# Performance work log

Hardware: AMD Instinct MI355X
Metric: run time of the kernel (lower is better)

The kernel has to match this reference:

```python
import jax, jax.numpy as jnp
import numpy as np

DICT_LEN = 9
NUM_LS = 8
DIM = 1024
SEQ = 2048
BZ = 32


def setup_inputs() -> dict:
    key = jax.random.key(0)
    k_x, k_ids, k_w, k_b = jax.random.split(key, 4)
    x = jax.random.normal(k_x, (SEQ, BZ, DIM), dtype=jnp.float32)
    lang_ids = jax.random.randint(k_ids, (BZ,), 0, DICT_LEN)
    # torch nn.Linear init: U(-1/sqrt(in), 1/sqrt(in)), weight shape [out, in]
    bound = 1.0 / np.sqrt(DIM)
    W = jax.random.uniform(k_w, (NUM_LS, DIM, DIM), dtype=jnp.float32, minval=-bound, maxval=bound)
    b = jax.random.uniform(k_b, (NUM_LS, DIM), dtype=jnp.float32, minval=-bound, maxval=bound)
    return {"x": x, "lang_ids": lang_ids, "W": W, "b": b}


def reference(x, lang_ids, W, b):
    # Mapper.forward: gid = dict_len - 1 - lang_ids; tokens with gid in [1, num_ls]
    # are transformed by Linear #(gid-1); all other batch columns pass through.
    gid = DICT_LEN - 1 - lang_ids                      # [bz]
    active = (gid >= 1) & (gid <= NUM_LS)              # [bz]
    eidx = jnp.clip(gid - 1, 0, NUM_LS - 1)            # [bz] expert index (dummy 0 where inactive)
    We = W[eidx]                                       # [bz, dim, dim] (torch Linear weight layout [out, in])
    be = b[eidx]                                       # [bz, dim]
    y = jnp.einsum("sbd,bed->sbe", x, We) + be[None, :, :]
    return jnp.where(active[None, :, None], y, x)
```

## Files before the change

kernel.cpp:

```cpp
#include <hip/hip_runtime.h>
#include <hip/hip_bf16.h>

#define TSEQ 2048
#define TBZ  32
#define TDIM 1024
#define NLS  8

typedef __attribute__((ext_vector_type(8))) short bf16x8;
typedef __attribute__((ext_vector_type(4))) float f32x4;

__device__ inline unsigned int pk2(float lo, float hi) {
    __hip_bfloat162 h = __float22bfloat162_rn(make_float2(lo, hi));
    return *reinterpret_cast<const unsigned int*>(&h);
}

__device__ inline void gload_lds16(const void* g, void* l) {
    __builtin_amdgcn_global_load_lds(
        (const __attribute__((address_space(1))) unsigned int*)g,
        (__attribute__((address_space(3))) unsigned int*)l,
        16, 0, 0);
}

__global__ __launch_bounds__(256) void conv_x(const float* __restrict__ x,
                                              unsigned short* __restrict__ xb) {
    const int total = TSEQ * TBZ * TDIM / 8;
    const int stride = gridDim.x * 256;
    for (int i = blockIdx.x * 256 + threadIdx.x; i < total; i += stride) {
        const int d8  = i & (TDIM / 8 - 1);
        const int row = i >> 7;
        const int s   = row >> 5;
        const int b   = row & (TBZ - 1);
        const float* src = x + (long)row * TDIM + d8 * 8;
        f32x4 v0 = *(const f32x4*)(src);
        f32x4 v1 = *(const f32x4*)(src + 4);
        uint4 o;
        o.x = pk2(v0.x, v0.y); o.y = pk2(v0.z, v0.w);
        o.z = pk2(v1.x, v1.y); o.w = pk2(v1.z, v1.w);
        *(uint4*)(xb + (long)(b * TSEQ + s) * TDIM + d8 * 8) = o;
    }
}

__global__ __launch_bounds__(256) void conv_w(const float* __restrict__ W,
                                              unsigned short* __restrict__ wb) {
    const int total = NLS * TDIM * TDIM / 8;
    const int stride = gridDim.x * 256;
    for (int i = blockIdx.x * 256 + threadIdx.x; i < total; i += stride) {
        const float* src = W + (long)i * 8;
        f32x4 v0 = *(const f32x4*)(src);
        f32x4 v1 = *(const f32x4*)(src + 4);
        uint4 o;
        o.x = pk2(v0.x, v0.y); o.y = pk2(v0.z, v0.w);
        o.z = pk2(v1.x, v1.y); o.w = pk2(v1.z, v1.w);
        *(uint4*)(wb + (long)i * 8) = o;
    }
}


#define BAR __builtin_amdgcn_s_barrier()
#define LGKM asm volatile("s_waitcnt lgkmcnt(0)" ::: "memory")
#define VMC(n) asm volatile("s_waitcnt vmcnt(" #n ")" ::: "memory")

__global__ __launch_bounds__(512, 2) void mapper_gemm8(
    const unsigned short* __restrict__ xb,
    const int* __restrict__ lang_ids,
    const unsigned short* __restrict__ wb,
    const float* __restrict__ bias,
    const float* __restrict__ x,
    float* __restrict__ out)
{
    const int p  = blockIdx.x;
    const int l  = (p & 7) * 128 + (p >> 3);
    const int b  = l >> 5;
    const int mt = (l >> 2) & 7;
    const int nt = l & 3;
    const int s0 = mt * 256;
    const int e0 = nt * 256;
    const int tid = threadIdx.x;

    const int gid = 8 - lang_ids[b];
    const bool active = (gid >= 1) && (gid <= 8);
    int eb = gid - 1; eb = eb < 0 ? 0 : (eb > 7 ? 7 : eb);

    if (!active) {
        const f32x4* xs = (const f32x4*)x;
        f32x4*       os = (f32x4*)out;
        const int rs4 = TBZ * TDIM / 4;
        for (int i = tid; i < 256 * 256 / 4; i += 512) {
            int r = i >> 6;
            int c = i & 63;
            long idx = (long)(s0 + r) * rs4 + b * (TDIM / 4) + (e0 >> 2) + c;
            os[idx] = xs[idx];
        }
        return;
    }

    __shared__ uint4 ldsbuf[131072 / 16];
    char* ldsc = (char*)ldsbuf;

    const int lane = tid & 63;
    const int wave = tid >> 6;
    const int wr   = wave >> 2;
    const int wc   = wave & 3;
    const int fr   = lane & 15;
    const int fq   = lane >> 4;
    const int fr7  = fr & 7;

    const unsigned short* __restrict__ Aab = xb + (long)b  * TSEQ * TDIM + (long)s0 * TDIM;
    const unsigned short* __restrict__ Bbb = wb + (long)eb * TDIM * TDIM + (long)e0 * TDIM;

    const int L    = lane;
    const int lch8 = ((L & 7) ^ (L >> 3)) * 8;
    const int ldA0 = wave * 2048 + L * 16;
    const unsigned short* aG[2][2];
    const unsigned short* bG[2][2];
    #pragma unroll
    for (int j = 0; j < 2; ++j) {
        const int rr = wave * 16 + j * 8 + (L >> 3);
        #pragma unroll
        for (int mh = 0; mh < 2; ++mh)
            aG[j][mh] = Aab + ((rr >> 6) * 128 + mh * 64 + (rr & 63)) * TDIM + lch8;
        #pragma unroll
        for (int nh = 0; nh < 2; ++nh)
            bG[j][nh] = Bbb + ((rr >> 5) * 64 + nh * 32 + (rr & 31)) * TDIM + lch8;
    }

#define STAGE_A(slot, mh, kofs) do { \
    gload_lds16(aG[0][mh] + (kofs), ldsc + (slot)*32768 + (mh)*16384 + ldA0); \
    gload_lds16(aG[1][mh] + (kofs), ldsc + (slot)*32768 + (mh)*16384 + ldA0 + 1024); \
} while (0)
#define STAGE_B(slot, nh, kofs) do { \
    gload_lds16(bG[0][nh] + (kofs), ldsc + 65536 + (slot)*32768 + (nh)*16384 + ldA0); \
    gload_lds16(bG[1][nh] + (kofs), ldsc + 65536 + (slot)*32768 + (nh)*16384 + ldA0 + 1024); \
} while (0)
#define RD_A(slot, mh) do { \
    _Pragma("unroll") for (int ml = 0; ml < 4; ++ml) { \
        const int rr = wr * 64 + ml * 16 + fr; \
        _Pragma("unroll") for (int kk = 0; kk < 2; ++kk) \
            af[ml][kk] = *(const bf16x8*)(ldsc + (slot)*32768 + (mh)*16384 + rr*128 + (((kk*4+fq) ^ fr7) << 4)); \
    } } while (0)
#define RD_B(slot, nh, br) do { \
    _Pragma("unroll") for (int nl = 0; nl < 2; ++nl) { \
        const int rr = wc * 32 + nl * 16 + fr; \
        _Pragma("unroll") for (int kk = 0; kk < 2; ++kk) \
            br[nl][kk] = *(const bf16x8*)(ldsc + 65536 + (slot)*32768 + (nh)*16384 + rr*128 + (((kk*4+fq) ^ fr7) << 4)); \
    } } while (0)
#define MM(mh, nh, br) do { \
    __builtin_amdgcn_s_setprio(1); \
    _Pragma("unroll") for (int ml = 0; ml < 4; ++ml) \
    _Pragma("unroll") for (int nl = 0; nl < 2; ++nl) \
    _Pragma("unroll") for (int kk = 0; kk < 2; ++kk) \
        acc[(mh)*4+ml][(nh)*2+nl] = __builtin_amdgcn_mfma_f32_16x16x32_bf16( \
            af[ml][kk], br[nl][kk], acc[(mh)*4+ml][(nh)*2+nl], 0, 0, 0); \
    __builtin_amdgcn_s_setprio(0); \
} while (0)

    f32x4 acc[8][4];
    #pragma unroll
    for (int m = 0; m < 8; ++m)
        #pragma unroll
        for (int n = 0; n < 4; ++n)
            acc[m][n] = (f32x4){0.f, 0.f, 0.f, 0.f};

    bf16x8 af[4][2], bf0[2][2], bf1[2][2];

    STAGE_A(0, 0, 0);  STAGE_B(0, 0, 0);  STAGE_B(0, 1, 0);  STAGE_A(0, 1, 0);
    STAGE_A(1, 0, 64); STAGE_B(1, 0, 64); STAGE_B(1, 1, 64);
    VMC(6); BAR;

    for (int it = 0; it < 7; ++it) {
        const int ka = it * 128;
        const int kb = ka + 64;
        const int kn = ka + 128;
        const int km = ka + 192;
        RD_A(0, 0); RD_B(0, 0, bf0); STAGE_A(1, 1, kb);
        BAR; LGKM; MM(0, 0, bf0); BAR;
        RD_B(0, 1, bf1); STAGE_A(0, 0, kn);
        BAR; LGKM; MM(0, 1, bf1); BAR;
        RD_A(0, 1); STAGE_B(0, 0, kn);
        BAR; LGKM; MM(1, 0, bf0); BAR;
        STAGE_B(0, 1, kn);
        BAR; MM(1, 1, bf1); VMC(6); BAR;
        RD_A(1, 0); RD_B(1, 0, bf0); STAGE_A(0, 1, kn);
        BAR; LGKM; MM(0, 0, bf0); BAR;
        RD_B(1, 1, bf1); STAGE_A(1, 0, km);
        BAR; LGKM; MM(0, 1, bf1); BAR;
        RD_A(1, 1); STAGE_B(1, 0, km);
        BAR; LGKM; MM(1, 0, bf0); BAR;
        STAGE_B(1, 1, km);
        BAR; MM(1, 1, bf1); VMC(6); BAR;
    }
    {
        const int kb = 7 * 128 + 64;
        RD_A(0, 0); RD_B(0, 0, bf0); STAGE_A(1, 1, kb);
        BAR; LGKM; MM(0, 0, bf0); BAR;
        RD_B(0, 1, bf1);
        BAR; LGKM; MM(0, 1, bf1); BAR;
        RD_A(0, 1);
        BAR; LGKM; MM(1, 0, bf0); BAR;
        BAR; MM(1, 1, bf1); VMC(0); BAR;
        RD_A(1, 0); RD_B(1, 0, bf0);
        BAR; LGKM; MM(0, 0, bf0); BAR;
        RD_B(1, 1, bf1);
        BAR; LGKM; MM(0, 1, bf1); BAR;
        RD_A(1, 1);
        BAR; LGKM; MM(1, 0, bf0); BAR;
        BAR; MM(1, 1, bf1);
    }

    const int cr = lane >> 4;
    const int cc = lane & 15;
    #pragma unroll
    for (int n = 0; n < 4; ++n) {
        const int e  = e0 + wc * 64 + n * 16 + cc;
        const float bv = bias[eb * TDIM + e];
        #pragma unroll
        for (int m = 0; m < 8; ++m) {
            #pragma unroll
            for (int j = 0; j < 4; ++j) {
                const int s = s0 + wr * 128 + m * 16 + cr * 4 + j;
                out[(long)s * (TBZ * TDIM) + b * TDIM + e] = acc[m][n][j] + bv;
            }
        }
    }
#undef STAGE_A
#undef STAGE_B
#undef RD_A
#undef RD_B
#undef MM
}

__device__ inline unsigned short f2bf(float f) {
    union { float f; unsigned int u; } v; v.f = f;
    unsigned int r = v.u + 0x7fffu + ((v.u >> 16) & 1u);
    return (unsigned short)(r >> 16);
}
constexpr int FLDS = 40;

__global__ __launch_bounds__(256) void mapper_fused(
    const float* __restrict__ x, const int* __restrict__ lang_ids,
    const float* __restrict__ W, const float* __restrict__ bias,
    float* __restrict__ out)
{
    const int bid = blockIdx.x;
    const int b   = bid >> 7;
    const int t   = bid & 127;
    const int mt  = t >> 3;
    const int nt  = t & 7;
    const int s0  = mt * 128;
    const int e0  = nt * 128;
    const int tid = threadIdx.x;

    const int gid = 8 - lang_ids[b];
    const bool active = (gid >= 1) && (gid <= 8);
    int eb = gid - 1; eb = eb < 0 ? 0 : (eb > 7 ? 7 : eb);

    if (!active) {
        const f32x4* xs = (const f32x4*)x;
        f32x4*       os = (f32x4*)out;
        const int rs4 = TBZ * TDIM / 4;
        for (int i = tid; i < 128 * 128 / 4; i += 256) {
            int r = i >> 5, c = i & 31;
            long idx = (long)(s0 + r) * rs4 + b * (TDIM / 4) + (e0 >> 2) + c;
            os[idx] = xs[idx];
        }
        return;
    }

    __shared__ unsigned short As[128 * FLDS];
    __shared__ unsigned short Bs[128 * FLDS];
    const float* __restrict__ Wb = W + (long)eb * TDIM * TDIM;

    const int lane = tid & 63;
    const int wave = tid >> 6;
    const int wrr  = wave >> 1;
    const int wcc  = wave & 1;

    f32x4 acc[4][4];
    #pragma unroll
    for (int m = 0; m < 4; ++m)
        #pragma unroll
        for (int n = 0; n < 4; ++n)
            acc[m][n] = (f32x4){0.f, 0.f, 0.f, 0.f};

    const int rg = tid >> 3;
    const int cg = tid & 7;
    const int fr = lane & 15;
    const int fo = (lane >> 4) * 8;

    for (int k0 = 0; k0 < TDIM; k0 += 32) {
        __syncthreads();
        #pragma unroll
        for (int pp = 0; pp < 4; ++pp) {
            const int r = rg + pp * 32;
            f32x4 av = *(const f32x4*)(x  + (long)(s0 + r) * (TBZ * TDIM) + b * TDIM + k0 + cg * 4);
            f32x4 bv = *(const f32x4*)(Wb + (long)(e0 + r) * TDIM + k0 + cg * 4);
            unsigned int alo = (unsigned)f2bf(av.x) | ((unsigned)f2bf(av.y) << 16);
            unsigned int ahi = (unsigned)f2bf(av.z) | ((unsigned)f2bf(av.w) << 16);
            unsigned int blo = (unsigned)f2bf(bv.x) | ((unsigned)f2bf(bv.y) << 16);
            unsigned int bhi = (unsigned)f2bf(bv.z) | ((unsigned)f2bf(bv.w) << 16);
            *(uint2*)&As[r * FLDS + cg * 4] = make_uint2(alo, ahi);
            *(uint2*)&Bs[r * FLDS + cg * 4] = make_uint2(blo, bhi);
        }
        __syncthreads();

        bf16x8 af2[4], bfm[4];
        #pragma unroll
        for (int m = 0; m < 4; ++m)
            af2[m] = *(const bf16x8*)&As[(wrr * 64 + m * 16 + fr) * FLDS + fo];
        #pragma unroll
        for (int n = 0; n < 4; ++n)
            bfm[n] = *(const bf16x8*)&Bs[(wcc * 64 + n * 16 + fr) * FLDS + fo];
        #pragma unroll
        for (int m = 0; m < 4; ++m)
            #pragma unroll
            for (int n = 0; n < 4; ++n)
                acc[m][n] = __builtin_amdgcn_mfma_f32_16x16x32_bf16(af2[m], bfm[n], acc[m][n], 0, 0, 0);
    }

    const int cr = lane >> 4;
    const int cc = lane & 15;
    #pragma unroll
    for (int n = 0; n < 4; ++n) {
        const int e  = e0 + wcc * 64 + n * 16 + cc;
        const float bv = bias[eb * TDIM + e];
        #pragma unroll
        for (int m = 0; m < 4; ++m) {
            #pragma unroll
            for (int j = 0; j < 4; ++j) {
                const int s = s0 + wrr * 64 + m * 16 + cr * 4 + j;
                out[(long)s * (TBZ * TDIM) + b * TDIM + e] = acc[m][n][j] + bv;
            }
        }
    }
}

extern "C" void kernel_launch(void* const* d_in, const int* in_sizes, int n_in,
                              void* d_out, int out_size, void* d_ws, size_t ws_size,
                              hipStream_t stream) {
    const float* x        = (const float*)d_in[0];
    const int*   lang_ids = (const int*)d_in[1];
    const float* W        = (const float*)d_in[2];
    const float* bias     = (const float*)d_in[3];
    float*       out      = (float*)d_out;

    const size_t xbytes = (size_t)TSEQ * TBZ * TDIM * 2;
    const size_t wbytes = (size_t)NLS * TDIM * TDIM * 2;

    if (ws_size >= xbytes + wbytes) {
        unsigned short* xbp = (unsigned short*)d_ws;
        unsigned short* wbp = (unsigned short*)((char*)d_ws + xbytes);
        conv_x<<<4096, 256, 0, stream>>>(x, xbp);
        conv_w<<<2048, 256, 0, stream>>>(W, wbp);
        mapper_gemm8<<<TBZ * 8 * 4, 512, 0, stream>>>(xbp, lang_ids, wbp, bias, x, out);
    } else {
        mapper_fused<<<TBZ * 16 * 8, 256, 0, stream>>>(x, lang_ids, W, bias, out);
    }
}
```

Before: 272.4 us.

## Merge conversion kernels, move passthrough copy into conversion, make GEMM blocks persistent over two tiles

Combines the x and W bf16 conversion kernels into one launch. The conversion of x now writes passthrough rows for inactive batch columns straight to the output instead of converting them, so the GEMM kernel just returns for inactive columns. The GEMM launches half as many blocks, and each one processes two 256-row M tiles back to back, streaming K continuously across both via a combined offset macro. This removes one launch and the pipeline drain and refill between tiles. The cost is longer-running blocks, less parallelism across the grid, and extra index arithmetic for the combined offsets.

New measurement: 271.4 us. Within noise of the previous version (-0.4%).

```diff
diff --git a/kernel.cpp b/kernel.cpp
--- a/kernel.cpp
+++ b/kernel.cpp
@@ -21,37 +21,49 @@
         16, 0, 0);
 }
 
-__global__ __launch_bounds__(256) void conv_x(const float* __restrict__ x,
-                                              unsigned short* __restrict__ xb) {
+__global__ __launch_bounds__(256) void conv_all(
+    const float* __restrict__ x, const int* __restrict__ lang_ids,
+    const float* __restrict__ W,
+    unsigned short* __restrict__ xb, unsigned short* __restrict__ wb,
+    float* __restrict__ out)
+{
+    const int bid = blockIdx.x;
+    if (bid < 512) {
+        const int total = NLS * TDIM * TDIM / 8;
+        const int stride = 512 * 256;
+        for (int i = bid * 256 + threadIdx.x; i < total; i += stride) {
+            const float* src = W + (long)i * 8;
+            f32x4 v0 = *(const f32x4*)(src);
+            f32x4 v1 = *(const f32x4*)(src + 4);
+            uint4 o;
+            o.x = pk2(v0.x, v0.y); o.y = pk2(v0.z, v0.w);
+            o.z = pk2(v1.x, v1.y); o.w = pk2(v1.z, v1.w);
+            *(uint4*)(wb + (long)i * 8) = o;
+        }
+        return;
+    }
+    const int xbid = bid - 512;
     const int total = TSEQ * TBZ * TDIM / 8;
-    const int stride = gridDim.x * 256;
-    for (int i = blockIdx.x * 256 + threadIdx.x; i < total; i += stride) {
+    const int stride = 4096 * 256;
+    for (int i = xbid * 256 + threadIdx.x; i < total; i += stride) {
         const int d8  = i & (TDIM / 8 - 1);
         const int row = i >> 7;
-        const int s   = row >> 5;
         const int b   = row & (TBZ - 1);
+        const int gid = 8 - lang_ids[b];
         const float* src = x + (long)row * TDIM + d8 * 8;
         f32x4 v0 = *(const f32x4*)(src);
         f32x4 v1 = *(const f32x4*)(src + 4);
-        uint4 o;
-        o.x = pk2(v0.x, v0.y); o.y = pk2(v0.z, v0.w);
-        o.z = pk2(v1.x, v1.y); o.w = pk2(v1.z, v1.w);
-        *(uint4*)(xb + (long)(b * TSEQ + s) * TDIM + d8 * 8) = o;
-    }
-}
-
-__global__ __launch_bounds__(256) void conv_w(const float* __restrict__ W,
-                                              unsigned short* __restrict__ wb) {
-    const int total = NLS * TDIM * TDIM / 8;
-    const int stride = gridDim.x * 256;
-    for (int i = blockIdx.x * 256 + threadIdx.x; i < total; i += stride) {
-        const float* src = W + (long)i * 8;
-        f32x4 v0 = *(const f32x4*)(src);
-        f32x4 v1 = *(const f32x4*)(src + 4);
-        uint4 o;
-        o.x = pk2(v0.x, v0.y); o.y = pk2(v0.z, v0.w);
-        o.z = pk2(v1.x, v1.y); o.w = pk2(v1.z, v1.w);
-        *(uint4*)(wb + (long)i * 8) = o;
+        if (gid >= 1 && gid <= 8) {
+            const int s = row >> 5;
+            uint4 o;
+            o.x = pk2(v0.x, v0.y); o.y = pk2(v0.z, v0.w);
+            o.z = pk2(v1.x, v1.y); o.w = pk2(v1.z, v1.w);
+            *(uint4*)(xb + (long)(b * TSEQ + s) * TDIM + d8 * 8) = o;
+        } else {
+            float* dst = out + (long)row * TDIM + d8 * 8;
+            *(f32x4*)(dst)     = v0;
+            *(f32x4*)(dst + 4) = v1;
+        }
     }
 }
 
@@ -59,40 +71,28 @@
 #define BAR __builtin_amdgcn_s_barrier()
 #define LGKM asm volatile("s_waitcnt lgkmcnt(0)" ::: "memory")
 #define VMC(n) asm volatile("s_waitcnt vmcnt(" #n ")" ::: "memory")
-
-__global__ __launch_bounds__(512, 2) void mapper_gemm8(
+#define KAo(kv) (((kv) & 1023) + (((kv) >> 10) << 18))
+#define KBo(kv) ((kv) & 1023)
+
+__global__ __launch_bounds__(512, 2) void mapper_gemm8p(
     const unsigned short* __restrict__ xb,
     const int* __restrict__ lang_ids,
     const unsigned short* __restrict__ wb,
     const float* __restrict__ bias,
-    const float* __restrict__ x,
     float* __restrict__ out)
 {
     const int p  = blockIdx.x;
-    const int l  = (p & 7) * 128 + (p >> 3);
-    const int b  = l >> 5;
-    const int mt = (l >> 2) & 7;
+    const int l  = (p & 7) * 64 + (p >> 3);
+    const int b  = l >> 4;
+    const int strip = (l >> 2) & 3;
     const int nt = l & 3;
-    const int s0 = mt * 256;
+    const int s0 = strip * 512;
     const int e0 = nt * 256;
     const int tid = threadIdx.x;
 
     const int gid = 8 - lang_ids[b];
-    const bool active = (gid >= 1) && (gid <= 8);
-    int eb = gid - 1; eb = eb < 0 ? 0 : (eb > 7 ? 7 : eb);
-
-    if (!active) {
-        const f32x4* xs = (const f32x4*)x;
-        f32x4*       os = (f32x4*)out;
-        const int rs4 = TBZ * TDIM / 4;
-        for (int i = tid; i < 256 * 256 / 4; i += 512) {
-            int r = i >> 6;
-            int c = i & 63;
-            long idx = (long)(s0 + r) * rs4 + b * (TDIM / 4) + (e0 >> 2) + c;
-            os[idx] = xs[idx];
-        }
-        return;
-    }
+    if (!(gid >= 1 && gid <= 8)) return;
+    const int eb = gid - 1;
 
     __shared__ uint4 ldsbuf[131072 / 16];
     char* ldsc = (char*)ldsbuf;
@@ -167,60 +167,52 @@
     STAGE_A(1, 0, 64); STAGE_B(1, 0, 64); STAGE_B(1, 1, 64);
     VMC(6); BAR;
 
-    for (int it = 0; it < 7; ++it) {
-        const int ka = it * 128;
-        const int kb = ka + 64;
-        const int kn = ka + 128;
-        const int km = ka + 192;
-        RD_A(0, 0); RD_B(0, 0, bf0); STAGE_A(1, 1, kb);
-        BAR; LGKM; MM(0, 0, bf0); BAR;
-        RD_B(0, 1, bf1); STAGE_A(0, 0, kn);
-        BAR; LGKM; MM(0, 1, bf1); BAR;
-        RD_A(0, 1); STAGE_B(0, 0, kn);
-        BAR; LGKM; MM(1, 0, bf0); BAR;
-        STAGE_B(0, 1, kn);
-        BAR; MM(1, 1, bf1); VMC(6); BAR;
-        RD_A(1, 0); RD_B(1, 0, bf0); STAGE_A(0, 1, kn);
-        BAR; LGKM; MM(0, 0, bf0); BAR;
-        RD_B(1, 1, bf1); STAGE_A(1, 0, km);
-        BAR; LGKM; MM(0, 1, bf1); BAR;
-        RD_A(1, 1); STAGE_B(1, 0, km);
-        BAR; LGKM; MM(1, 0, bf0); BAR;
-        STAGE_B(1, 1, km);
-        BAR; MM(1, 1, bf1); VMC(6); BAR;
-    }
-    {
-        const int kb = 7 * 128 + 64;
-        RD_A(0, 0); RD_B(0, 0, bf0); STAGE_A(1, 1, kb);
-        BAR; LGKM; MM(0, 0, bf0); BAR;
-        RD_B(0, 1, bf1);
-        BAR; LGKM; MM(0, 1, bf1); BAR;
-        RD_A(0, 1);
-        BAR; LGKM; MM(1, 0, bf0); BAR;
-        BAR; MM(1, 1, bf1); VMC(0); BAR;
-        RD_A(1, 0); RD_B(1, 0, bf0);
-        BAR; LGKM; MM(0, 0, bf0); BAR;
-        RD_B(1, 1, bf1);
-        BAR; LGKM; MM(0, 1, bf1); BAR;
-        RD_A(1, 1);
-        BAR; LGKM; MM(1, 0, bf0); BAR;
-        BAR; MM(1, 1, bf1);
-    }
-
     const int cr = lane >> 4;
     const int cc = lane & 15;
-    #pragma unroll
-    for (int n = 0; n < 4; ++n) {
-        const int e  = e0 + wc * 64 + n * 16 + cc;
-        const float bv = bias[eb * TDIM + e];
-        #pragma unroll
-        for (int m = 0; m < 8; ++m) {
+
+    for (int mtl = 0; mtl < 2; ++mtl) {
+        for (int it = 0; it < 8; ++it) {
+            const int kva = mtl * 1024 + it * 128;
+            const int kb = kva + 64;
+            const int kn = kva + 128;
+            const int km = kva + 192;
+            RD_A(0, 0); RD_B(0, 0, bf0); STAGE_A(1, 1, KAo(kb));
+            BAR; LGKM; MM(0, 0, bf0); BAR;
+            RD_B(0, 1, bf1); STAGE_A(0, 0, KAo(kn));
+            BAR; LGKM; MM(0, 1, bf1); BAR;
+            RD_A(0, 1); STAGE_B(0, 0, KBo(kn));
+            BAR; LGKM; MM(1, 0, bf0); BAR;
+            STAGE_B(0, 1, KBo(kn));
+            BAR; MM(1, 1, bf1); VMC(6); BAR;
+            RD_A(1, 0); RD_B(1, 0, bf0); STAGE_A(0, 1, KAo(kn));
+            BAR; LGKM; MM(0, 0, bf0); BAR;
+            RD_B(1, 1, bf1); STAGE_A(1, 0, KAo(km));
+            BAR; LGKM; MM(0, 1, bf1); BAR;
+            RD_A(1, 1); STAGE_B(1, 0, KBo(km));
+            BAR; LGKM; MM(1, 0, bf0); BAR;
+            STAGE_B(1, 1, KBo(km));
+            BAR; MM(1, 1, bf1); VMC(6); BAR;
+        }
+
+        const int sb = s0 + mtl * 256 + wr * 128;
+        #pragma unroll
+        for (int n = 0; n < 4; ++n) {
+            const int e  = e0 + wc * 64 + n * 16 + cc;
+            const float bv = bias[eb * TDIM + e];
             #pragma unroll
-            for (int j = 0; j < 4; ++j) {
-                const int s = s0 + wr * 128 + m * 16 + cr * 4 + j;
-                out[(long)s * (TBZ * TDIM) + b * TDIM + e] = acc[m][n][j] + bv;
+            for (int m = 0; m < 8; ++m) {
+                #pragma unroll
+                for (int j = 0; j < 4; ++j) {
+                    const int s = sb + m * 16 + cr * 4 + j;
+                    out[(long)s * (TBZ * TDIM) + b * TDIM + e] = acc[m][n][j] + bv;
+                }
             }
         }
+        #pragma unroll
+        for (int m = 0; m < 8; ++m)
+            #pragma unroll
+            for (int n = 0; n < 4; ++n)
+                acc[m][n] = (f32x4){0.f, 0.f, 0.f, 0.f};
     }
 #undef STAGE_A
 #undef STAGE_B
@@ -349,9 +341,8 @@
     if (ws_size >= xbytes + wbytes) {
         unsigned short* xbp = (unsigned short*)d_ws;
         unsigned short* wbp = (unsigned short*)((char*)d_ws + xbytes);
-        conv_x<<<4096, 256, 0, stream>>>(x, xbp);
-        conv_w<<<2048, 256, 0, stream>>>(W, wbp);
-        mapper_gemm8<<<TBZ * 8 * 4, 512, 0, stream>>>(xbp, lang_ids, wbp, bias, x, out);
+        conv_all<<<4608, 256, 0, stream>>>(x, lang_ids, W, xbp, wbp, out);
+        mapper_gemm8p<<<512, 512, 0, stream>>>(xbp, lang_ids, wbp, bias, out);
     } else {
         mapper_fused<<<TBZ * 16 * 8, 256, 0, stream>>>(x, lang_ids, W, bias, out);
     }
```
